# Kernel optimization log

Hardware: AMD Instinct MI355X
Metric: run time of the kernel (lower is better)

## Reference

```python
import jax, jax.numpy as jnp
import numpy as np

D_MODEL = 1024
N_HEADS = 16
D_EXP = 4
B, SQ, SKV = 2, 2048, 2048
LN_EPS = 1e-5


def _linear_params(key, d_in, d_out):
    kw, kb = jax.random.split(key)
    w = jax.random.normal(kw, (d_in, d_out), jnp.float32) * 0.02  # stored [in,out]
    b = jax.random.normal(kb, (d_out,), jnp.float32) * 0.02
    return w, b


def setup_inputs() -> dict:
    key = jax.random.key(0)
    ks = jax.random.split(key, 16)
    inp = {}
    inp["x"] = jax.random.normal(ks[0], (B, SQ, D_MODEL), jnp.float32)
    inp["encoder_out"] = jax.random.normal(ks[1], (B, SKV, D_MODEL), jnp.float32)
    # causal target mask, broadcast over batch and heads
    inp["tgt_mask"] = jnp.tril(jnp.ones((SQ, SQ), jnp.int32))[None, None]
    inp["src_mask"] = jnp.ones((1, 1, SQ, SKV), jnp.int32)
    # self-attention params
    inp["wq_s"], inp["bq_s"] = _linear_params(ks[2], D_MODEL, D_MODEL)
    inp["wk_s"], inp["bk_s"] = _linear_params(ks[3], D_MODEL, D_MODEL)
    inp["wv_s"], inp["bv_s"] = _linear_params(ks[4], D_MODEL, D_MODEL)
    inp["wo_s"], inp["bo_s"] = _linear_params(ks[5], D_MODEL, D_MODEL)
    # cross-attention params
    inp["wq_c"], inp["bq_c"] = _linear_params(ks[6], D_MODEL, D_MODEL)
    inp["wk_c"], inp["bk_c"] = _linear_params(ks[7], D_MODEL, D_MODEL)
    inp["wv_c"], inp["bv_c"] = _linear_params(ks[8], D_MODEL, D_MODEL)
    inp["wo_c"], inp["bo_c"] = _linear_params(ks[9], D_MODEL, D_MODEL)
    # feedforward params
    inp["ff1_w"], inp["ff1_b"] = _linear_params(ks[10], D_MODEL, D_MODEL * D_EXP)
    inp["ff2_w"], inp["ff2_b"] = _linear_params(ks[11], D_MODEL * D_EXP, D_MODEL)
    # layernorm params (3 AddNorms)
    for i, k in zip((1, 2, 3), (ks[12], ks[13], ks[14])):
        inp[f"ln{i}_g"] = jnp.ones((D_MODEL,), jnp.float32)
        inp[f"ln{i}_b"] = jnp.zeros((D_MODEL,), jnp.float32)
    return inp


def _layernorm(x, g, b):
    mu = jnp.mean(x, axis=-1, keepdims=True)
    var = jnp.mean(jnp.square(x - mu), axis=-1, keepdims=True)
    return (x - mu) / jnp.sqrt(var + LN_EPS) * g + b


def _mha(xq, xkv, wq, bq, wk, bk, wv, bv, wo, bo, mask):
    Bq, Sq, D = xq.shape
    Hd = D // N_HEADS
    q = (xq @ wq + bq).reshape(Bq, Sq, N_HEADS, Hd).transpose(0, 2, 1, 3)   # bhqd
    k = (xkv @ wk + bk).reshape(Bq, -1, N_HEADS, Hd).transpose(0, 2, 1, 3)  # bhkd
    v = (xkv @ wv + bv).reshape(Bq, -1, N_HEADS, Hd).transpose(0, 2, 1, 3)  # bhkd
    score = jnp.einsum("bhqd,bhkd->bhqk", q, k) / jnp.sqrt(jnp.float32(Hd))
    score = jnp.where(mask == 0, -jnp.inf, score)
    attn = jax.nn.softmax(score, axis=-1)
    ctx = jnp.einsum("bhqk,bhkd->bhqd", attn, v)
    ctx = ctx.transpose(0, 2, 1, 3).reshape(Bq, Sq, D)
    return ctx @ wo + bo


def reference(x, encoder_out, tgt_mask, src_mask,
              wq_s, bq_s, wk_s, bk_s, wv_s, bv_s, wo_s, bo_s,
              wq_c, bq_c, wk_c, bk_c, wv_c, bv_c, wo_c, bo_c,
              ff1_w, ff1_b, ff2_w, ff2_b,
              ln1_g, ln1_b, ln2_g, ln2_b, ln3_g, ln3_b):
    # dropout is identity in eval mode
    sa = _mha(x, x, wq_s, bq_s, wk_s, bk_s, wv_s, bv_s, wo_s, bo_s, tgt_mask)
    h = _layernorm(x + sa, ln1_g, ln1_b)
    ca = _mha(h, encoder_out, wq_c, bq_c, wk_c, bk_c, wv_c, bv_c, wo_c, bo_c, src_mask)
    h2 = _layernorm(h + ca, ln2_g, ln2_b)
    ff = jax.nn.relu(h2 @ ff1_w + ff1_b) @ ff2_w + ff2_b
    return _layernorm(h2 + ff, ln3_g, ln3_b)
```

## Files before the change

### kernel.cpp

```cpp
#include <hip/hip_runtime.h>
#include <stdint.h>

typedef __bf16 bf16;
typedef __attribute__((ext_vector_type(4))) float f32x4;
typedef __attribute__((ext_vector_type(8))) __bf16 bf16x8;
typedef __attribute__((ext_vector_type(4))) __bf16 bf16x4;

#define DM   1024
#define NH   16
#define HDIM 64
#define BB   2
#define SEQ  2048
#define MR   (BB * SEQ)
#define DFF  4096
#define MEG  (1024 * 1024)

__global__ void detect_kernel(const unsigned int* __restrict__ xw,
                              int* __restrict__ flag) {
  int tid = threadIdx.x;
  int bad = 0;
  for (int i = tid; i < 4096; i += 64) {
    unsigned int w = xw[i];
    float flo = __uint_as_float((w & 0xffffu) << 16);
    if (!(fabsf(flo) < 100.f)) bad = 1;
  }
  unsigned long long m = __ballot(bad);
  if (tid == 0) *flag = (m == 0ull) ? 1 : 0;
}

__global__ __launch_bounds__(256) void cvt_big_kernel(
    const void* __restrict__ src, bf16* __restrict__ dst, int n4,
    const int* __restrict__ flag) {
  int i = blockIdx.x * 256 + threadIdx.x;
  if (i >= n4) return;
  if (*flag) {
    ((bf16x4*)dst)[i] = ((const bf16x4*)src)[i];
  } else {
    float4 v = ((const float4*)src)[i];
    bf16x4 o = {(bf16)v.x, (bf16)v.y, (bf16)v.z, (bf16)v.w};
    ((bf16x4*)dst)[i] = o;
  }
}

struct P16 { const void* p[16]; };
__global__ __launch_bounds__(256) void cvt_small_kernel(
    P16 ps, bf16* __restrict__ dstbase, const int* __restrict__ flag) {
  const int ncnt[16] = {1024,1024,1024,1024,1024,1024,1024,1024,
                        4096,1024,1024,1024,1024,1024,1024,1024};
  const int doff[16] = {0,1024,2048,3072,4096,5120,6144,7168,
                        8192,12288,13312,14336,15360,16384,17408,18432};
  int b = blockIdx.x;
  int n = ncnt[b];
  bool isbf = (*flag) != 0;
  const void* s = ps.p[b];
  bf16* d = dstbase + doff[b];
  for (int i = threadIdx.x; i * 4 < n; i += 256) {
    if (isbf) {
      ((bf16x4*)d)[i] = ((const bf16x4*)s)[i];
    } else {
      float4 v = ((const float4*)s)[i];
      bf16x4 o = {(bf16)v.x, (bf16)v.y, (bf16)v.z, (bf16)v.w};
      ((bf16x4*)d)[i] = o;
    }
  }
}

static __device__ __forceinline__ void gl_lds16(const bf16* g, bf16* l) {
  auto gp = reinterpret_cast<__attribute__((address_space(1))) unsigned int*>(
      reinterpret_cast<uintptr_t>(g));
  auto lp = reinterpret_cast<__attribute__((address_space(3))) unsigned int*>(
      (unsigned int)reinterpret_cast<uintptr_t>(l));
  __builtin_amdgcn_global_load_lds(gp, lp, 16, 0, 0);
}

struct WTB {
  const void* src[10];
  int dstoff[10];
  int K[10], N[10];
  int bstart[10];
};
__global__ __launch_bounds__(256) void wt_all_kernel(WTB wb, bf16* __restrict__ wtbase,
                                                     const int* __restrict__ flag) {
  __shared__ bf16 tile[32][33];
  int bid = blockIdx.x;
  int wi = 0;
  while (wi < 9 && bid >= wb.bstart[wi + 1]) ++wi;
  int rel = bid - wb.bstart[wi];
  int N = wb.N[wi], K = wb.K[wi];
  int nb = N >> 5;
  int n0 = (rel % nb) * 32, k0 = (rel / nb) * 32;
  const void* w = wb.src[wi];
  bf16* wt = wtbase + wb.dstoff[wi];
  bool isbf = (*flag) != 0;
  int tid = threadIdx.x;
  int tx = tid & 31, ty = tid >> 5;
#pragma unroll
  for (int i = 0; i < 4; ++i) {
    size_t idx = (size_t)(k0 + ty + i * 8) * N + n0 + tx;
    tile[ty + i * 8][tx] = isbf ? ((const bf16*)w)[idx]
                                : (bf16)(((const float*)w)[idx]);
  }
  __syncthreads();
#pragma unroll
  for (int i = 0; i < 4; ++i)
    wt[(size_t)(n0 + ty + i * 8) * K + k0 + tx] = tile[tx][ty + i * 8];
}

template <int TM>
__global__ __launch_bounds__(256) void gemm_kernel(
    const bf16* __restrict__ A, const bf16* __restrict__ Bt,
    const bf16* __restrict__ bias, bf16* __restrict__ outb,
    int M, int N, int K, int relu) {
  constexpr int NI = TM / 32;
  constexpr int WM = TM / 2;
  constexpr int CA = TM / 64;
  __shared__ alignas(16) bf16 As[TM * 32];
  __shared__ alignas(16) bf16 Bs[128 * 32];
  int tid = threadIdx.x;
  int lane = tid & 63, wv = tid >> 6;
  int quad = lane >> 4, l15 = lane & 15;
  int m0 = blockIdx.y * TM, n0 = blockIdx.x * 128;
  int wm = wv >> 1, wn = wv & 1;

  f32x4 acc[NI][4];
#pragma unroll
  for (int i = 0; i < NI; ++i)
#pragma unroll
    for (int j = 0; j < 4; ++j) acc[i][j] = (f32x4){0.f, 0.f, 0.f, 0.f};

  int sr = lane >> 2, sc = (lane & 3) * 8;
  const bf16* gA[CA];
  bf16* lA[CA];
#pragma unroll
  for (int t = 0; t < CA; ++t) {
    int ch = wv * CA + t;
    gA[t] = A + (size_t)(m0 + ch * 16 + sr) * K + sc;
    lA[t] = As + ch * 512 + lane * 8;
  }
  const bf16* gB0 = Bt + (size_t)(n0 + (wv * 2) * 16 + sr) * K + sc;
  const bf16* gB1 = Bt + (size_t)(n0 + (wv * 2 + 1) * 16 + sr) * K + sc;
  bf16* lB0 = Bs + (wv * 2) * 512 + lane * 8;
  bf16* lB1 = Bs + (wv * 2 + 1) * 512 + lane * 8;

  for (int k0 = 0; k0 < K; k0 += 32) {
#pragma unroll
    for (int t = 0; t < CA; ++t) gl_lds16(gA[t] + k0, lA[t]);
    gl_lds16(gB0 + k0, lB0);
    gl_lds16(gB1 + k0, lB1);
    __syncthreads();
    bf16x8 af[NI], bfr[4];
#pragma unroll
    for (int i = 0; i < NI; ++i)
      af[i] = *(const bf16x8*)(As + (wm * WM + i * 16 + l15) * 32 + quad * 8);
#pragma unroll
    for (int j = 0; j < 4; ++j)
      bfr[j] = *(const bf16x8*)(Bs + (wn * 64 + j * 16 + l15) * 32 + quad * 8);
#pragma unroll
    for (int i = 0; i < NI; ++i)
#pragma unroll
      for (int j = 0; j < 4; ++j)
        acc[i][j] = __builtin_amdgcn_mfma_f32_16x16x32_bf16(af[i], bfr[j],
                                                            acc[i][j], 0, 0, 0);
    __syncthreads();
  }

#pragma unroll
  for (int j = 0; j < 4; ++j) {
    int col = n0 + wn * 64 + j * 16 + l15;
    float bval = (float)bias[col];
#pragma unroll
    for (int i = 0; i < NI; ++i) {
      int rb = m0 + wm * WM + i * 16 + quad * 4;
#pragma unroll
      for (int r = 0; r < 4; ++r) {
        float v = acc[i][j][r] + bval;
        if (relu) v = fmaxf(v, 0.f);
        outb[(size_t)(rb + r) * N + col] = (bf16)v;
      }
    }
  }
}

__global__ __launch_bounds__(256) void gemm_splitk_kernel(
    const bf16* __restrict__ A, const bf16* __restrict__ Bt,
    float* __restrict__ pout, int M, int N, int KC, int Ktot) {
  __shared__ alignas(16) bf16 As[128 * 32];
  __shared__ alignas(16) bf16 Bs[128 * 32];
  int tid = threadIdx.x;
  int lane = tid & 63, wv = tid >> 6;
  int quad = lane >> 4, l15 = lane & 15;
  int m0 = blockIdx.y * 128, n0 = blockIdx.x * 128;
  int wm = wv >> 1, wn = wv & 1;
  int kb = blockIdx.z * KC;
  pout += (size_t)blockIdx.z * M * N;

  f32x4 acc[4][4];
#pragma unroll
  for (int i = 0; i < 4; ++i)
#pragma unroll
    for (int j = 0; j < 4; ++j) acc[i][j] = (f32x4){0.f, 0.f, 0.f, 0.f};

  int sr = lane >> 2, sc = (lane & 3) * 8;
  const bf16* gA0 = A + (size_t)(m0 + (wv * 2) * 16 + sr) * Ktot + sc;
  const bf16* gA1 = A + (size_t)(m0 + (wv * 2 + 1) * 16 + sr) * Ktot + sc;
  const bf16* gB0 = Bt + (size_t)(n0 + (wv * 2) * 16 + sr) * Ktot + sc;
  const bf16* gB1 = Bt + (size_t)(n0 + (wv * 2 + 1) * 16 + sr) * Ktot + sc;
  bf16* lA0 = As + (wv * 2) * 512 + lane * 8;
  bf16* lA1 = As + (wv * 2 + 1) * 512 + lane * 8;
  bf16* lB0 = Bs + (wv * 2) * 512 + lane * 8;
  bf16* lB1 = Bs + (wv * 2 + 1) * 512 + lane * 8;

  for (int k0 = kb; k0 < kb + KC; k0 += 32) {
    gl_lds16(gA0 + k0, lA0);
    gl_lds16(gA1 + k0, lA1);
    gl_lds16(gB0 + k0, lB0);
    gl_lds16(gB1 + k0, lB1);
    __syncthreads();
    bf16x8 af[4], bfr[4];
#pragma unroll
    for (int i = 0; i < 4; ++i)
      af[i] = *(const bf16x8*)(As + (wm * 64 + i * 16 + l15) * 32 + quad * 8);
#pragma unroll
    for (int j = 0; j < 4; ++j)
      bfr[j] = *(const bf16x8*)(Bs + (wn * 64 + j * 16 + l15) * 32 + quad * 8);
#pragma unroll
    for (int i = 0; i < 4; ++i)
#pragma unroll
      for (int j = 0; j < 4; ++j)
        acc[i][j] = __builtin_amdgcn_mfma_f32_16x16x32_bf16(af[i], bfr[j],
                                                            acc[i][j], 0, 0, 0);
    __syncthreads();
  }
#pragma unroll
  for (int j = 0; j < 4; ++j) {
    int col = n0 + wn * 64 + j * 16 + l15;
#pragma unroll
    for (int i = 0; i < 4; ++i) {
      int rb = m0 + wm * 64 + i * 16 + quad * 4;
#pragma unroll
      for (int r = 0; r < 4; ++r)
        pout[(size_t)(rb + r) * N + col] = acc[i][j][r];
    }
  }
}

__global__ __launch_bounds__(256) void vt_pre_kernel(
    const bf16* __restrict__ v, int vstride, bf16* __restrict__ vt, int skv) {
  __shared__ bf16 tile[32][33];
  int tid = threadIdx.x;
  int tx = tid & 31, ty = tid >> 5;
  int kv0 = blockIdx.x * 32, d0 = blockIdx.y * 32;
  int bh = blockIdx.z;
  int b = bh >> 4, h = bh & 15;
  const bf16* src = v + (size_t)b * skv * vstride + h * HDIM;
#pragma unroll
  for (int i = 0; i < 4; ++i)
    tile[ty + i * 8][tx] = src[(size_t)(kv0 + ty + i * 8) * vstride + d0 + tx];
  __syncthreads();
  bf16* dst = vt + ((size_t)bh * HDIM + d0) * skv + kv0;
#pragma unroll
  for (int i = 0; i < 4; ++i)
    dst[(size_t)(ty + i * 8) * skv + tx] = tile[tx][ty + i * 8];
}

__global__ __launch_bounds__(256) void flash7_kernel(
    const bf16* __restrict__ Q, int qstride,
    const bf16* __restrict__ Kk, int kstride,
    const bf16* __restrict__ VT, bf16* __restrict__ ctx,
    float* __restrict__ opart, float* __restrict__ lpart,
    int skv, int causal, int nsplit) {
  __shared__ alignas(16) bf16 Kt[64 * 72];
  __shared__ alignas(16) bf16 Vt[64 * 72];
  __shared__ alignas(16) bf16 Pt[4][32 * 72];
  int tid = threadIdx.x;
  int lane = tid & 63, wv = tid >> 6, quad = lane >> 4, l15 = lane & 15;
  int qb = blockIdx.x, h = blockIdx.y;
  int zz = blockIdx.z;
  int b = zz / nsplit;
  int half = zz - b * nsplit;
  int q0 = qb * 128;
  int qw = q0 + wv * 32;

  bf16x8 qf[2][2];
  const float qsc = 0.125f * 1.44269504f;
#pragma unroll
  for (int a = 0; a < 2; ++a) {
    const bf16* qp = Q + (size_t)(b * SEQ + qw + a * 16 + l15) * qstride + h * HDIM;
    qf[a][0] = *(const bf16x8*)(qp + quad * 8);
    qf[a][1] = *(const bf16x8*)(qp + 32 + quad * 8);
#pragma unroll
    for (int j = 0; j < 8; ++j) {
      qf[a][0][j] = (bf16)((float)qf[a][0][j] * qsc);
      qf[a][1][j] = (bf16)((float)qf[a][1][j] * qsc);
    }
  }
  bf16x8 onesf;
#pragma unroll
  for (int j = 0; j < 8; ++j) onesf[j] = (l15 == 0) ? (bf16)1.0f : (bf16)0.0f;

  f32x4 o[2][4], oL[2];
#pragma unroll
  for (int a = 0; a < 2; ++a) {
    oL[a] = (f32x4){0.f, 0.f, 0.f, 0.f};
#pragma unroll
    for (int j = 0; j < 4; ++j) o[a][j] = (f32x4){0.f, 0.f, 0.f, 0.f};
  }

  int nch_tot = causal ? (q0 + 128) / 64 : skv / 64;
  int c_lo = (half * nch_tot) / nsplit;
  int c_hi = ((half + 1) * nch_tot) / nsplit;
  int srow = tid >> 2, sseg = (tid & 3) * 16;
  const bf16* kg = Kk + (size_t)b * skv * kstride + (size_t)srow * kstride +
                   h * HDIM + sseg;
  const bf16* vg = VT + ((size_t)(b * NH + h) * HDIM + srow) * skv + sseg;

  bf16x8 k0r, k1r, v0r, v1r;
  if (c_lo < c_hi) {
    const bf16* kp = kg + (size_t)(c_lo * 64) * kstride;
    const bf16* vp = vg + c_lo * 64;
    k0r = *(const bf16x8*)(kp);
    k1r = *(const bf16x8*)(kp + 8);
    v0r = *(const bf16x8*)(vp);
    v1r = *(const bf16x8*)(vp + 8);
  }

  for (int c = c_lo; c < c_hi; ++c) {
    int kv0 = c * 64;
    __syncthreads();
    *(bf16x8*)(&Kt[srow * 72 + sseg]) = k0r;
    *(bf16x8*)(&Kt[srow * 72 + sseg + 8]) = k1r;
    *(bf16x8*)(&Vt[srow * 72 + sseg]) = v0r;
    *(bf16x8*)(&Vt[srow * 72 + sseg + 8]) = v1r;
    if (c + 1 < c_hi) {
      const bf16* kn = kg + (size_t)(kv0 + 64) * kstride;
      const bf16* vn = vg + kv0 + 64;
      k0r = *(const bf16x8*)(kn);
      k1r = *(const bf16x8*)(kn + 8);
      v0r = *(const bf16x8*)(vn);
      v1r = *(const bf16x8*)(vn + 8);
    }
    __syncthreads();

    if (!causal || kv0 <= qw + 31) {
      f32x4 s[2][4];
#pragma unroll
      for (int t = 0; t < 4; ++t) {
        bf16x8 kt0 = *(const bf16x8*)(&Kt[(t * 16 + l15) * 72 + quad * 8]);
        bf16x8 kt1 = *(const bf16x8*)(&Kt[(t * 16 + l15) * 72 + 32 + quad * 8]);
#pragma unroll
        for (int a = 0; a < 2; ++a) {
          f32x4 z = (f32x4){0.f, 0.f, 0.f, 0.f};
          z = __builtin_amdgcn_mfma_f32_16x16x32_bf16(kt0, qf[a][0], z, 0, 0, 0);
          z = __builtin_amdgcn_mfma_f32_16x16x32_bf16(kt1, qf[a][1], z, 0, 0, 0);
          s[a][t] = z;
        }
      }
      if (causal && kv0 + 63 > qw) {
#pragma unroll
        for (int a = 0; a < 2; ++a)
#pragma unroll
          for (int t = 0; t < 4; ++t)
#pragma unroll
            for (int r = 0; r < 4; ++r)
              if (kv0 + t * 16 + quad * 4 + r > qw + a * 16 + l15)
                s[a][t][r] = -1e30f;
      }
#pragma unroll
      for (int a = 0; a < 2; ++a)
#pragma unroll
        for (int t = 0; t < 4; ++t) {
          bf16x4 pk;
#pragma unroll
          for (int r = 0; r < 4; ++r) pk[r] = (bf16)exp2f(s[a][t][r]);
          *(bf16x4*)(&Pt[wv][(a * 16 + l15) * 72 + t * 16 + quad * 4]) = pk;
        }
      __asm__ volatile("s_waitcnt lgkmcnt(0)" ::: "memory");
      bf16x8 pf[2][2];
#pragma unroll
      for (int a = 0; a < 2; ++a) {
        pf[a][0] = *(const bf16x8*)(&Pt[wv][(a * 16 + l15) * 72 + quad * 8]);
        pf[a][1] = *(const bf16x8*)(&Pt[wv][(a * 16 + l15) * 72 + 32 + quad * 8]);
      }
#pragma unroll
      for (int a = 0; a < 2; ++a) {
        oL[a] = __builtin_amdgcn_mfma_f32_16x16x32_bf16(pf[a][0], onesf, oL[a], 0, 0, 0);
        oL[a] = __builtin_amdgcn_mfma_f32_16x16x32_bf16(pf[a][1], onesf, oL[a], 0, 0, 0);
      }
#pragma unroll
      for (int j = 0; j < 4; ++j) {
        bf16x8 bv0 = *(const bf16x8*)(&Vt[(j * 16 + l15) * 72 + quad * 8]);
        bf16x8 bv1 = *(const bf16x8*)(&Vt[(j * 16 + l15) * 72 + 32 + quad * 8]);
#pragma unroll
        for (int a = 0; a < 2; ++a) {
          o[a][j] = __builtin_amdgcn_mfma_f32_16x16x32_bf16(pf[a][0], bv0, o[a][j], 0, 0, 0);
          o[a][j] = __builtin_amdgcn_mfma_f32_16x16x32_bf16(pf[a][1], bv1, o[a][j], 0, 0, 0);
        }
      }
    }
  }

  if (nsplit == 1) {
#pragma unroll
    for (int a = 0; a < 2; ++a)
#pragma unroll
      for (int r = 0; r < 4; ++r) {
        float l = __shfl(oL[a][r], quad * 16, 64);
        float inv = 1.0f / fmaxf(l, 1e-30f);
        bf16* cp = ctx + (size_t)(b * SEQ + qw + a * 16 + quad * 4 + r) * DM + h * HDIM;
#pragma unroll
        for (int j = 0; j < 4; ++j) cp[j * 16 + l15] = (bf16)(o[a][j][r] * inv);
      }
  } else {
    float* op = opart + (size_t)half * MR * DM;
#pragma unroll
    for (int a = 0; a < 2; ++a)
#pragma unroll
      for (int r = 0; r < 4; ++r) {
        float* cp = op + (size_t)(b * SEQ + qw + a * 16 + quad * 4 + r) * DM + h * HDIM;
#pragma unroll
        for (int j = 0; j < 4; ++j) cp[j * 16 + l15] = o[a][j][r];
      }
    if (l15 == 0) {
#pragma unroll
      for (int a = 0; a < 2; ++a)
#pragma unroll
        for (int r = 0; r < 4; ++r)
          lpart[(size_t)((half * BB + b) * NH + h) * SEQ + qw + a * 16 + quad * 4 + r] =
              oL[a][r];
    }
  }
}

template <int NS>
__global__ __launch_bounds__(256) void flash_comb_kernel(
    const float* __restrict__ opart, const float* __restrict__ lpart,
    bf16* __restrict__ ctx) {
  int row = blockIdx.x, tid = threadIdx.x;
  int b = row >> 11, q = row & (SEQ - 1);
  int h = tid >> 4;
  float l = 0.f;
#pragma unroll
  for (int s = 0; s < NS; ++s)
    l += lpart[(size_t)((s * BB + b) * NH + h) * SEQ + q];
  float inv = 1.0f / fmaxf(l, 1e-30f);
  float a0 = 0.f, a1 = 0.f, a2 = 0.f, a3 = 0.f;
#pragma unroll
  for (int s = 0; s < NS; ++s) {
    f32x4 v = ((const f32x4*)(opart + (size_t)s * MR * DM + (size_t)row * DM))[tid];
    a0 += v[0]; a1 += v[1]; a2 += v[2]; a3 += v[3];
  }
  bf16x4 ob = {(bf16)(a0 * inv), (bf16)(a1 * inv),
               (bf16)(a2 * inv), (bf16)(a3 * inv)};
  ((bf16x4*)(ctx + (size_t)row * DM))[tid] = ob;
}

template <int NP>
__global__ __launch_bounds__(256) void addnorm_red_kernel(
    const bf16* __restrict__ res, const float* __restrict__ part,
    const bf16* __restrict__ bias, const bf16* __restrict__ g,
    const bf16* __restrict__ be, bf16* __restrict__ yb,
    void* __restrict__ outAny, const int* __restrict__ flag) {
  int row = blockIdx.x, tid = threadIdx.x;
  float a0 = 0.f, a1 = 0.f, a2 = 0.f, a3 = 0.f;
#pragma unroll
  for (int p = 0; p < NP; ++p) {
    float4 v = ((const float4*)(part + (size_t)p * MR * DM + (size_t)row * DM))[tid];
    a0 += v.x; a1 += v.y; a2 += v.z; a3 += v.w;
  }
  bf16x4 bb = ((const bf16x4*)bias)[tid];
  bf16x4 rr = ((const bf16x4*)(res + (size_t)row * DM))[tid];
  float s0 = (float)rr[0] + a0 + (float)bb[0];
  float s1 = (float)rr[1] + a1 + (float)bb[1];
  float s2 = (float)rr[2] + a2 + (float)bb[2];
  float s3 = (float)rr[3] + a3 + (float)bb[3];
  float sum = s0 + s1 + s2 + s3;
  float sq = s0 * s0 + s1 * s1 + s2 * s2 + s3 * s3;
#pragma unroll
  for (int mk = 32; mk >= 1; mk >>= 1) {
    sum += __shfl_xor(sum, mk, 64);
    sq += __shfl_xor(sq, mk, 64);
  }
  __shared__ float red[8];
  int wvi = tid >> 6, lane = tid & 63;
  if (lane == 0) { red[wvi * 2] = sum; red[wvi * 2 + 1] = sq; }
  __syncthreads();
  sum = red[0] + red[2] + red[4] + red[6];
  sq = red[1] + red[3] + red[5] + red[7];
  float mu = sum * (1.0f / DM);
  float var = sq * (1.0f / DM) - mu * mu;
  float rstd = rsqrtf(var + 1e-5f);
  bf16x4 g4 = ((const bf16x4*)g)[tid];
  bf16x4 b4 = ((const bf16x4*)be)[tid];
  float y0 = (s0 - mu) * rstd * (float)g4[0] + (float)b4[0];
  float y1 = (s1 - mu) * rstd * (float)g4[1] + (float)b4[1];
  float y2 = (s2 - mu) * rstd * (float)g4[2] + (float)b4[2];
  float y3 = (s3 - mu) * rstd * (float)g4[3] + (float)b4[3];
  if (yb) {
    bf16x4 ob = {(bf16)y0, (bf16)y1, (bf16)y2, (bf16)y3};
    ((bf16x4*)(yb + (size_t)row * DM))[tid] = ob;
  }
  if (outAny) {
    if (*flag) {
      bf16x4 ob = {(bf16)y0, (bf16)y1, (bf16)y2, (bf16)y3};
      ((bf16x4*)outAny)[(size_t)row * 256 + tid] = ob;
    } else {
      ((float4*)outAny)[(size_t)row * 256 + tid] = make_float4(y0, y1, y2, y3);
    }
  }
}

extern "C" void kernel_launch(void* const* d_in, const int* in_sizes, int n_in,
                              void* d_out, int out_size, void* d_ws, size_t ws_size,
                              hipStream_t stream) {
  (void)in_sizes; (void)n_in; (void)out_size; (void)ws_size;
  const void* x_raw   = d_in[0];
  const void* enc_raw = d_in[1];

  char* ws = (char*)d_ws;
  size_t off = 0;
  auto alloc = [&](size_t bytes) -> void* {
    void* p = ws + off;
    off += (bytes + 255) & ~(size_t)255;
    return p;
  };
  const size_t SB = (size_t)MR * DM;
  int* flag    = (int*)alloc(256);
  bf16* smallb = (bf16*)alloc(20480 * 2);
  bf16* wt   = (bf16*)alloc((size_t)16 * MEG * 2);
  bf16* xb   = (bf16*)alloc(SB * 2);
  bf16* encb = (bf16*)alloc(SB * 2);
  bf16* vtg  = (bf16*)alloc(SB * 2);
  bf16* ctx  = (bf16*)alloc(SB * 2);
  bf16* hb1  = (bf16*)alloc(SB * 2);
  bf16* hb2  = (bf16*)alloc(SB * 2);
  bf16* qkv  = (bf16*)alloc(SB * 3 * 2);
  bf16* kvc  = (bf16*)alloc(SB * 2 * 2);
  float* part = (float*)alloc(SB * 4 * 4);
  float* lpart = (float*)alloc((size_t)3 * BB * NH * SEQ * 4);
  bf16* gbuf = qkv;
  bf16* qc   = xb;

  bf16* b_qkvs = smallb + 0;     bf16* b_os  = smallb + 3072;
  bf16* b_qc   = smallb + 4096;  bf16* b_kvc = smallb + 5120;
  bf16* b_oc   = smallb + 7168;  bf16* b_f1  = smallb + 8192;
  bf16* b_f2   = smallb + 12288;
  bf16* l1g = smallb + 13312; bf16* l1b = smallb + 14336;
  bf16* l2g = smallb + 15360; bf16* l2b = smallb + 16384;
  bf16* l3g = smallb + 17408; bf16* l3b = smallb + 18432;

  detect_kernel<<<1, 64, 0, stream>>>((const unsigned int*)x_raw, flag);
  cvt_big_kernel<<<(int)(SB / 1024), 256, 0, stream>>>(x_raw, xb, (int)(SB / 4), flag);
  cvt_big_kernel<<<(int)(SB / 1024), 256, 0, stream>>>(enc_raw, encb, (int)(SB / 4), flag);
  P16 ps;
  ps.p[0] = d_in[5];  ps.p[1] = d_in[7];  ps.p[2] = d_in[9];  ps.p[3] = d_in[11];
  ps.p[4] = d_in[13]; ps.p[5] = d_in[15]; ps.p[6] = d_in[17]; ps.p[7] = d_in[19];
  ps.p[8] = d_in[21]; ps.p[9] = d_in[23];
  ps.p[10] = d_in[24]; ps.p[11] = d_in[25]; ps.p[12] = d_in[26];
  ps.p[13] = d_in[27]; ps.p[14] = d_in[28]; ps.p[15] = d_in[29];
  cvt_small_kernel<<<16, 256, 0, stream>>>(ps, smallb, flag);

  WTB wb;
  const int wsrc[10] = {4, 6, 8, 10, 12, 14, 16, 18, 20, 22};
  for (int i = 0; i < 10; ++i) {
    wb.src[i] = d_in[wsrc[i]];
    wb.K[i] = 1024; wb.N[i] = 1024;
    wb.dstoff[i] = i * MEG;
    wb.bstart[i] = i * 1024;
  }
  wb.N[8] = 4096;
  wb.K[9] = 4096; wb.dstoff[9] = 12 * MEG;
  wb.bstart[9] = 8192 + 4096;
  wt_all_kernel<<<16384, 256, 0, stream>>>(wb, wt, flag);

  gemm_kernel<128><<<dim3(24, 32), 256, 0, stream>>>(xb, wt, b_qkvs, qkv,
                                                     MR, 3072, DM, 0);
  vt_pre_kernel<<<dim3(SEQ / 32, 2, 32), 256, 0, stream>>>(qkv + 2048, 3072, vtg, SEQ);
  flash7_kernel<<<dim3(SEQ / 128, NH, BB * 3), 256, 0, stream>>>(
      qkv, 3072, qkv + 1024, 3072, vtg, ctx, part, lpart, SEQ, 1, 3);
  flash_comb_kernel<3><<<MR, 256, 0, stream>>>(part, lpart, ctx);
  gemm_splitk_kernel<<<dim3(8, 32, 2), 256, 0, stream>>>(
      ctx, wt + (size_t)3 * MEG, part, MR, DM, 512, DM);
  addnorm_red_kernel<2><<<MR, 256, 0, stream>>>(xb, part, b_os, l1g, l1b,
                                                hb1, nullptr, flag);
  gemm_kernel<64><<<dim3(8, 64), 256, 0, stream>>>(hb1, wt + (size_t)4 * MEG,
                                                   b_qc, qc, MR, DM, DM, 0);
  gemm_kernel<128><<<dim3(16, 32), 256, 0, stream>>>(encb, wt + (size_t)5 * MEG,
                                                     b_kvc, kvc, MR, 2048, DM, 0);
  vt_pre_kernel<<<dim3(SEQ / 32, 2, 32), 256, 0, stream>>>(kvc + 1024, 2048, vtg, SEQ);
  flash7_kernel<<<dim3(SEQ / 128, NH, BB * 3), 256, 0, stream>>>(
      qc, 1024, kvc, 2048, vtg, ctx, part, lpart, SEQ, 0, 3);
  flash_comb_kernel<3><<<MR, 256, 0, stream>>>(part, lpart, ctx);
  gemm_splitk_kernel<<<dim3(8, 32, 2), 256, 0, stream>>>(
      ctx, wt + (size_t)7 * MEG, part, MR, DM, 512, DM);
  addnorm_red_kernel<2><<<MR, 256, 0, stream>>>(hb1, part, b_oc, l2g, l2b,
                                                hb2, nullptr, flag);
  gemm_kernel<128><<<dim3(32, 32), 256, 0, stream>>>(hb2, wt + (size_t)8 * MEG,
                                                     b_f1, gbuf, MR, DFF, DM, 1);
  gemm_splitk_kernel<<<dim3(8, 32, 4), 256, 0, stream>>>(
      gbuf, wt + (size_t)12 * MEG, part, MR, DM, 1024, DFF);
  addnorm_red_kernel<4><<<MR, 256, 0, stream>>>(hb2, part, b_f2, l3g, l3b,
                                                nullptr, d_out, flag);
}
```

Measured before the change: 677.4 us.

## Rewrite flash attention with async LDS double buffering and register-resident P

Replaces the flash attention kernel with a version that stages K and V^T tiles into double-buffered, XOR-swizzled shared memory via global_load_lds, removing the register round-trip and one barrier per chunk. The softmax probabilities stay in registers and feed 16x16x16 MFMAs directly instead of going through a shared-memory P buffer. Row sums come from an MFMA against a ones vector. Split-KV is reduced from 3 to 2 for self-attention and removed for cross-attention, dropping one combine kernel, at the cost of fewer blocks in flight and more serial work per block.

Measured after the change: 665.1 us. About the same (-1.8%).

```diff
diff --git a/kernel.cpp b/kernel.cpp
--- a/kernel.cpp
+++ b/kernel.cpp
@@ -5,6 +5,7 @@
 typedef __attribute__((ext_vector_type(4))) float f32x4;
 typedef __attribute__((ext_vector_type(8))) __bf16 bf16x8;
 typedef __attribute__((ext_vector_type(4))) __bf16 bf16x4;
+typedef __attribute__((ext_vector_type(4))) short s16x4;
 
 #define DM   1024
 #define NH   16
@@ -71,6 +72,12 @@
   auto lp = reinterpret_cast<__attribute__((address_space(3))) unsigned int*>(
       (unsigned int)reinterpret_cast<uintptr_t>(l));
   __builtin_amdgcn_global_load_lds(gp, lp, 16, 0, 0);
+}
+
+static __device__ __forceinline__ s16x4 as_s16x4(bf16x4 v) {
+  s16x4 r;
+  __builtin_memcpy(&r, &v, 8);
+  return r;
 }
 
 struct WTB {
@@ -263,15 +270,14 @@
     dst[(size_t)(ty + i * 8) * skv + tx] = tile[tx][ty + i * 8];
 }
 
-__global__ __launch_bounds__(256) void flash7_kernel(
+__global__ __launch_bounds__(256, 4) void flash8_kernel(
     const bf16* __restrict__ Q, int qstride,
     const bf16* __restrict__ Kk, int kstride,
     const bf16* __restrict__ VT, bf16* __restrict__ ctx,
     float* __restrict__ opart, float* __restrict__ lpart,
     int skv, int causal, int nsplit) {
-  __shared__ alignas(16) bf16 Kt[64 * 72];
-  __shared__ alignas(16) bf16 Vt[64 * 72];
-  __shared__ alignas(16) bf16 Pt[4][32 * 72];
+  __shared__ alignas(16) bf16 KTl[2][64 * 64];
+  __shared__ alignas(16) bf16 VTl[2][64 * 64];
   int tid = threadIdx.x;
   int lane = tid & 63, wv = tid >> 6, quad = lane >> 4, l15 = lane & 15;
   int qb = blockIdx.x, h = blockIdx.y;
@@ -280,6 +286,7 @@
   int half = zz - b * nsplit;
   int q0 = qb * 128;
   int qw = q0 + wv * 32;
+  int l7 = l15 & 7;
 
   bf16x8 qf[2][2];
   const float qsc = 0.125f * 1.44269504f;
@@ -294,9 +301,7 @@
       qf[a][1][j] = (bf16)((float)qf[a][1][j] * qsc);
     }
   }
-  bf16x8 onesf;
-#pragma unroll
-  for (int j = 0; j < 8; ++j) onesf[j] = (l15 == 0) ? (bf16)1.0f : (bf16)0.0f;
+  s16x4 onesA = {0x3F80, 0x3F80, 0x3F80, 0x3F80};
 
   f32x4 o[2][4], oL[2];
 #pragma unroll
@@ -309,124 +314,102 @@
   int nch_tot = causal ? (q0 + 128) / 64 : skv / 64;
   int c_lo = (half * nch_tot) / nsplit;
   int c_hi = ((half + 1) * nch_tot) / nsplit;
-  int srow = tid >> 2, sseg = (tid & 3) * 16;
-  const bf16* kg = Kk + (size_t)b * skv * kstride + (size_t)srow * kstride +
-                   h * HDIM + sseg;
-  const bf16* vg = VT + ((size_t)(b * NH + h) * HDIM + srow) * skv + sseg;
-
-  bf16x8 k0r, k1r, v0r, v1r;
-  if (c_lo < c_hi) {
-    const bf16* kp = kg + (size_t)(c_lo * 64) * kstride;
-    const bf16* vp = vg + c_lo * 64;
-    k0r = *(const bf16x8*)(kp);
-    k1r = *(const bf16x8*)(kp + 8);
-    v0r = *(const bf16x8*)(vp);
-    v1r = *(const bf16x8*)(vp + 8);
-  }
+
+  int l8 = lane >> 3;
+  int colseg = (lane & 7) ^ l8;
+  int grow = wv * 16 + l8;
+  const bf16* kbase = Kk + ((size_t)b * skv + grow) * kstride + h * HDIM + colseg * 8;
+  const bf16* vbase = VT + ((size_t)(b * NH + h) * HDIM + grow) * skv + colseg * 8;
+  bf16* kls = &KTl[0][wv * 1024];
+  bf16* vls = &VTl[0][wv * 1024];
+
+  auto STAGE = [&](int bb, int cc) {
+    const bf16* ks = kbase + (size_t)(cc * 64) * kstride;
+    const bf16* vs = vbase + cc * 64;
+    bf16* kd = kls + bb * 4096;
+    bf16* vd = vls + bb * 4096;
+    gl_lds16(ks, kd);
+    gl_lds16(ks + (size_t)8 * kstride, kd + 512);
+    gl_lds16(vs, vd);
+    gl_lds16(vs + (size_t)8 * skv, vd + 512);
+  };
+
+  if (c_lo < c_hi) STAGE(0, c_lo);
 
   for (int c = c_lo; c < c_hi; ++c) {
+    int cur = (c - c_lo) & 1;
     int kv0 = c * 64;
     __syncthreads();
-    *(bf16x8*)(&Kt[srow * 72 + sseg]) = k0r;
-    *(bf16x8*)(&Kt[srow * 72 + sseg + 8]) = k1r;
-    *(bf16x8*)(&Vt[srow * 72 + sseg]) = v0r;
-    *(bf16x8*)(&Vt[srow * 72 + sseg + 8]) = v1r;
-    if (c + 1 < c_hi) {
-      const bf16* kn = kg + (size_t)(kv0 + 64) * kstride;
-      const bf16* vn = vg + kv0 + 64;
-      k0r = *(const bf16x8*)(kn);
-      k1r = *(const bf16x8*)(kn + 8);
-      v0r = *(const bf16x8*)(vn);
-      v1r = *(const bf16x8*)(vn + 8);
-    }
-    __syncthreads();
+    if (c + 1 < c_hi) STAGE(cur ^ 1, c + 1);
 
     if (!causal || kv0 <= qw + 31) {
-      f32x4 s[2][4];
+      const bf16* kt_base = &KTl[0][0] + cur * 4096;
+      const bf16* vt_base = &VTl[0][0] + cur * 4096;
+      bf16x4 p[2][4];
 #pragma unroll
       for (int t = 0; t < 4; ++t) {
-        bf16x8 kt0 = *(const bf16x8*)(&Kt[(t * 16 + l15) * 72 + quad * 8]);
-        bf16x8 kt1 = *(const bf16x8*)(&Kt[(t * 16 + l15) * 72 + 32 + quad * 8]);
+        const bf16* kb = kt_base + (t * 16 + l15) * 64;
+        bf16x8 kt0 = *(const bf16x8*)(kb + ((quad ^ l7) << 3));
+        bf16x8 kt1 = *(const bf16x8*)(kb + (((quad + 4) ^ l7) << 3));
 #pragma unroll
         for (int a = 0; a < 2; ++a) {
           f32x4 z = (f32x4){0.f, 0.f, 0.f, 0.f};
           z = __builtin_amdgcn_mfma_f32_16x16x32_bf16(kt0, qf[a][0], z, 0, 0, 0);
           z = __builtin_amdgcn_mfma_f32_16x16x32_bf16(kt1, qf[a][1], z, 0, 0, 0);
-          s[a][t] = z;
+          if (causal && kv0 + 63 > qw) {
+#pragma unroll
+            for (int r = 0; r < 4; ++r)
+              if (kv0 + t * 16 + quad * 4 + r > qw + a * 16 + l15)
+                z[r] = -1e30f;
+          }
+          bf16x4 pk;
+#pragma unroll
+          for (int r = 0; r < 4; ++r) pk[r] = (bf16)exp2f(z[r]);
+          p[a][t] = pk;
+          oL[a] = __builtin_amdgcn_mfma_f32_16x16x16bf16_1k(
+              onesA, as_s16x4(pk), oL[a], 0, 0, 0);
         }
       }
-      if (causal && kv0 + 63 > qw) {
+#pragma unroll
+      for (int jt = 0; jt < 4; ++jt) {
+        const bf16* vb = vt_base + (jt * 16 + l15) * 64;
+        bf16x4 af[4];
+#pragma unroll
+        for (int t = 0; t < 4; ++t)
+          af[t] = *(const bf16x4*)(
+              vb + ((((t * 2 + (quad >> 1)) ^ l7) << 3) + ((quad & 1) << 2)));
 #pragma unroll
         for (int a = 0; a < 2; ++a)
 #pragma unroll
           for (int t = 0; t < 4; ++t)
-#pragma unroll
-            for (int r = 0; r < 4; ++r)
-              if (kv0 + t * 16 + quad * 4 + r > qw + a * 16 + l15)
-                s[a][t][r] = -1e30f;
+            o[a][jt] = __builtin_amdgcn_mfma_f32_16x16x16bf16_1k(
+                as_s16x4(af[t]), as_s16x4(p[a][t]), o[a][jt], 0, 0, 0);
       }
-#pragma unroll
-      for (int a = 0; a < 2; ++a)
-#pragma unroll
-        for (int t = 0; t < 4; ++t) {
-          bf16x4 pk;
-#pragma unroll
-          for (int r = 0; r < 4; ++r) pk[r] = (bf16)exp2f(s[a][t][r]);
-          *(bf16x4*)(&Pt[wv][(a * 16 + l15) * 72 + t * 16 + quad * 4]) = pk;
-        }
-      __asm__ volatile("s_waitcnt lgkmcnt(0)" ::: "memory");
-      bf16x8 pf[2][2];
-#pragma unroll
-      for (int a = 0; a < 2; ++a) {
-        pf[a][0] = *(const bf16x8*)(&Pt[wv][(a * 16 + l15) * 72 + quad * 8]);
-        pf[a][1] = *(const bf16x8*)(&Pt[wv][(a * 16 + l15) * 72 + 32 + quad * 8]);
+    }
+  }
+
+  if (nsplit == 1) {
+#pragma unroll
+    for (int a = 0; a < 2; ++a) {
+      float inv = 1.0f / fmaxf(oL[a][0], 1e-30f);
+      bf16* cp = ctx + (size_t)(b * SEQ + qw + a * 16 + l15) * DM + h * HDIM + quad * 4;
+#pragma unroll
+      for (int jt = 0; jt < 4; ++jt) {
+        bf16x4 ob = {(bf16)(o[a][jt][0] * inv), (bf16)(o[a][jt][1] * inv),
+                     (bf16)(o[a][jt][2] * inv), (bf16)(o[a][jt][3] * inv)};
+        *(bf16x4*)(cp + jt * 16) = ob;
       }
-#pragma unroll
-      for (int a = 0; a < 2; ++a) {
-        oL[a] = __builtin_amdgcn_mfma_f32_16x16x32_bf16(pf[a][0], onesf, oL[a], 0, 0, 0);
-        oL[a] = __builtin_amdgcn_mfma_f32_16x16x32_bf16(pf[a][1], onesf, oL[a], 0, 0, 0);
-      }
-#pragma unroll
-      for (int j = 0; j < 4; ++j) {
-        bf16x8 bv0 = *(const bf16x8*)(&Vt[(j * 16 + l15) * 72 + quad * 8]);
-        bf16x8 bv1 = *(const bf16x8*)(&Vt[(j * 16 + l15) * 72 + 32 + quad * 8]);
-#pragma unroll
-        for (int a = 0; a < 2; ++a) {
-          o[a][j] = __builtin_amdgcn_mfma_f32_16x16x32_bf16(pf[a][0], bv0, o[a][j], 0, 0, 0);
-          o[a][j] = __builtin_amdgcn_mfma_f32_16x16x32_bf16(pf[a][1], bv1, o[a][j], 0, 0, 0);
-        }
-      }
-    }
-  }
-
-  if (nsplit == 1) {
-#pragma unroll
-    for (int a = 0; a < 2; ++a)
-#pragma unroll
-      for (int r = 0; r < 4; ++r) {
-        float l = __shfl(oL[a][r], quad * 16, 64);
-        float inv = 1.0f / fmaxf(l, 1e-30f);
-        bf16* cp = ctx + (size_t)(b * SEQ + qw + a * 16 + quad * 4 + r) * DM + h * HDIM;
-#pragma unroll
-        for (int j = 0; j < 4; ++j) cp[j * 16 + l15] = (bf16)(o[a][j][r] * inv);
-      }
+    }
   } else {
-    float* op = opart + (size_t)half * MR * DM;
-#pragma unroll
-    for (int a = 0; a < 2; ++a)
-#pragma unroll
-      for (int r = 0; r < 4; ++r) {
-        float* cp = op + (size_t)(b * SEQ + qw + a * 16 + quad * 4 + r) * DM + h * HDIM;
-#pragma unroll
-        for (int j = 0; j < 4; ++j) cp[j * 16 + l15] = o[a][j][r];
-      }
-    if (l15 == 0) {
-#pragma unroll
-      for (int a = 0; a < 2; ++a)
-#pragma unroll
-        for (int r = 0; r < 4; ++r)
-          lpart[(size_t)((half * BB + b) * NH + h) * SEQ + qw + a * 16 + quad * 4 + r] =
-              oL[a][r];
+#pragma unroll
+    for (int a = 0; a < 2; ++a) {
+      float* op = opart + (size_t)half * MR * DM +
+                  (size_t)(b * SEQ + qw + a * 16 + l15) * DM + h * HDIM + quad * 4;
+#pragma unroll
+      for (int jt = 0; jt < 4; ++jt) *(f32x4*)(op + jt * 16) = o[a][jt];
+      if (lane < 16)
+        lpart[(size_t)((half * BB + b) * NH + h) * SEQ + qw + a * 16 + l15] =
+            oL[a][0];
     }
   }
 }
@@ -575,9 +558,9 @@
   gemm_kernel<128><<<dim3(24, 32), 256, 0, stream>>>(xb, wt, b_qkvs, qkv,
                                                      MR, 3072, DM, 0);
   vt_pre_kernel<<<dim3(SEQ / 32, 2, 32), 256, 0, stream>>>(qkv + 2048, 3072, vtg, SEQ);
-  flash7_kernel<<<dim3(SEQ / 128, NH, BB * 3), 256, 0, stream>>>(
-      qkv, 3072, qkv + 1024, 3072, vtg, ctx, part, lpart, SEQ, 1, 3);
-  flash_comb_kernel<3><<<MR, 256, 0, stream>>>(part, lpart, ctx);
+  flash8_kernel<<<dim3(SEQ / 128, NH, BB * 2), 256, 0, stream>>>(
+      qkv, 3072, qkv + 1024, 3072, vtg, ctx, part, lpart, SEQ, 1, 2);
+  flash_comb_kernel<2><<<MR, 256, 0, stream>>>(part, lpart, ctx);
   gemm_splitk_kernel<<<dim3(8, 32, 2), 256, 0, stream>>>(
       ctx, wt + (size_t)3 * MEG, part, MR, DM, 512, DM);
   addnorm_red_kernel<2><<<MR, 256, 0, stream>>>(xb, part, b_os, l1g, l1b,
@@ -587,9 +570,8 @@
   gemm_kernel<128><<<dim3(16, 32), 256, 0, stream>>>(encb, wt + (size_t)5 * MEG,
                                                      b_kvc, kvc, MR, 2048, DM, 0);
   vt_pre_kernel<<<dim3(SEQ / 32, 2, 32), 256, 0, stream>>>(kvc + 1024, 2048, vtg, SEQ);
-  flash7_kernel<<<dim3(SEQ / 128, NH, BB * 3), 256, 0, stream>>>(
-      qc, 1024, kvc, 2048, vtg, ctx, part, lpart, SEQ, 0, 3);
-  flash_comb_kernel<3><<<MR, 256, 0, stream>>>(part, lpart, ctx);
+  flash8_kernel<<<dim3(SEQ / 128, NH, BB), 256, 0, stream>>>(
+      qc, 1024, kvc, 2048, vtg, ctx, nullptr, nullptr, SEQ, 0, 1);
   gemm_splitk_kernel<<<dim3(8, 32, 2), 256, 0, stream>>>(
       ctx, wt + (size_t)7 * MEG, part, MR, DM, 512, DM);
   addnorm_red_kernel<2><<<MR, 256, 0, stream>>>(hb1, part, b_oc, l2g, l2b,
```
